# Kernel optimization log

Hardware: AMD Instinct MI355X
Metric: run time of the kernel (lower is better)

The kernel has to match this reference:

```python
import jax, jax.numpy as jnp
import numpy as np

B, T, C = 2, 2048, 2048
NH, NKV, D = 16, 4, 128
N_REP = NH // NKV
THETA = 10000.0


def setup_inputs() -> dict:
    key = jax.random.key(0)
    ks = jax.random.split(key, 5)
    s = 0.02
    return {
        "x": jax.random.normal(ks[0], (B, T, C), dtype=jnp.float32),
        "Wq": jax.random.normal(ks[1], (C, C), dtype=jnp.float32) * s,
        "Wk": jax.random.normal(ks[2], (NKV * D, C), dtype=jnp.float32) * s,
        "Wv": jax.random.normal(ks[3], (NKV * D, C), dtype=jnp.float32) * s,
        "Wo": jax.random.normal(ks[4], (C, C), dtype=jnp.float32) * s,
    }


def _rope(t):
    # t: (B, H, T, D); rotate pairs (even, odd) by angle pos * theta_i
    inv_freq = 1.0 / (THETA ** (jnp.arange(0, D, 2, dtype=jnp.float32) / D))  # (D/2,)
    ang = jnp.arange(T, dtype=jnp.float32)[:, None] * inv_freq[None, :]       # (T, D/2)
    cos, sin = jnp.cos(ang), jnp.sin(ang)
    te, to = t[..., 0::2], t[..., 1::2]
    re = te * cos - to * sin
    ro = te * sin + to * cos
    return jnp.stack([re, ro], axis=-1).reshape(t.shape).astype(t.dtype)


def reference(x, Wq, Wk, Wv, Wo):
    # Projections (Linear: y = x @ W.T)
    q = (x @ Wq.T).reshape(B, T, NH, D).transpose(0, 2, 1, 3)    # (B,NH,T,D)
    k = (x @ Wk.T).reshape(B, T, NKV, D).transpose(0, 2, 1, 3)   # (B,NKV,T,D)
    v = (x @ Wv.T).reshape(B, T, NKV, D).transpose(0, 2, 1, 3)
    q = _rope(q)
    k = _rope(k)
    # GQA: group query heads per kv head instead of materializing repeated K/V
    qg = q.reshape(B, NKV, N_REP, T, D)                          # (B,G,R,T,D)
    scale = 1.0 / jnp.sqrt(jnp.float32(D))
    scores = jnp.einsum("bgrtd,bgsd->bgrts", qg, k) * scale      # (B,G,R,T,T)
    causal = jnp.tril(jnp.ones((T, T), dtype=bool))
    scores = jnp.where(causal, scores, jnp.finfo(scores.dtype).min)
    attn = jax.nn.softmax(scores, axis=-1)
    out = jnp.einsum("bgrts,bgsd->bgrtd", attn, v)               # (B,G,R,T,D)
    out = out.reshape(B, NH, T, D).transpose(0, 2, 1, 3).reshape(B, T, C)
    return out @ Wo.T
```

## Files before the change

kernel.cpp:

```cpp
#include <hip/hip_runtime.h>
#include <hip/hip_bf16.h>
#include <stdint.h>

#define B_   2
#define T_   2048
#define C_   2048
#define NH_  16
#define NKV_ 4
#define D_   128
#define NREP_ 4

typedef __attribute__((ext_vector_type(8))) short bf16x8;
typedef __attribute__((ext_vector_type(4))) float f32x4;

__device__ inline short f2bs(float f) {
    __hip_bfloat16 h = __float2bfloat16(f);
    return *reinterpret_cast<short*>(&h);
}

__device__ inline void gl_lds16(const __hip_bfloat16* g, __hip_bfloat16* l) {
    __builtin_amdgcn_global_load_lds(
        (const __attribute__((address_space(1))) unsigned int*)g,
        (__attribute__((address_space(3))) unsigned int*)l,
        16, 0, 0);
}

__global__ void prep_kernel(const float* __restrict__ x,  const float* __restrict__ Wq,
                            const float* __restrict__ Wk, const float* __restrict__ Wv,
                            const float* __restrict__ Wo,
                            __hip_bfloat16* __restrict__ xb, __hip_bfloat16* __restrict__ wcat,
                            __hip_bfloat16* __restrict__ wob, float2* __restrict__ ropeTab) {
    int tid = blockIdx.x * blockDim.x + threadIdx.x;
    const int CVT_THREADS = 4718592;
    if (tid < CVT_THREADS) {
        int i4 = tid * 4;
        const float* src;
        __hip_bfloat16* dst;
        int off;
        if (i4 < 8388608)       { src = x;  dst = xb;             off = i4; }
        else if (i4 < 12582912) { src = Wq; dst = wcat;           off = i4 - 8388608; }
        else if (i4 < 13631488) { src = Wk; dst = wcat + 4194304; off = i4 - 12582912; }
        else if (i4 < 14680064) { src = Wv; dst = wcat + 5242880; off = i4 - 13631488; }
        else                    { src = Wo; dst = wob;            off = i4 - 14680064; }
        float4 v = *reinterpret_cast<const float4*>(src + off);
        short4 o;
        o.x = f2bs(v.x); o.y = f2bs(v.y); o.z = f2bs(v.z); o.w = f2bs(v.w);
        *reinterpret_cast<short4*>(dst + off) = o;
    } else {
        int e = tid - CVT_THREADS;
        if (e < 131072) {
            int t = e >> 6, p = e & 63;
            float inv = __expf(-(float)p * (9.210340371976184f / 64.0f));
            float ang = (float)t * inv;
            ropeTab[e] = make_float2(cosf(ang), sinf(ang));
        }
    }
}

__global__ __launch_bounds__(256) void gemm_qkv(const __hip_bfloat16* __restrict__ A,
                                                const __hip_bfloat16* __restrict__ Bm,
                                                const float2* __restrict__ ropeTab,
                                                __hip_bfloat16* __restrict__ qo,
                                                __hip_bfloat16* __restrict__ ko,
                                                __hip_bfloat16* __restrict__ vT) {
    const int K = 2048;
    __shared__ __hip_bfloat16 As[128 * 32];
    __shared__ __hip_bfloat16 Bs[128 * 32];
    const int tid  = threadIdx.x;
    const int lane = tid & 63;
    const int wv   = tid >> 6;
    const int m0 = blockIdx.y * 128, n0 = blockIdx.x * 128;
    const int wm = (wv >> 1) * 64, wn = (wv & 1) * 64;
    const int q16 = lane >> 4, r16 = lane & 15;

    f32x4 acc[4][4] = {};

    const int lrow = tid >> 2;
    const int lcol = (tid & 3) * 8;
    const __hip_bfloat16* aG = A  + (size_t)(m0 + lrow) * K + lcol;
    const __hip_bfloat16* bG = Bm + (size_t)(n0 + lrow) * K + lcol;
    __hip_bfloat16* aL = As + tid * 8;
    __hip_bfloat16* bL = Bs + tid * 8;

    for (int k0 = 0; k0 < K; k0 += 32) {
        __syncthreads();
        gl_lds16(aG + k0,          aL);
        gl_lds16(aG + 64 * K + k0, aL + 2048);
        gl_lds16(bG + k0,          bL);
        gl_lds16(bG + 64 * K + k0, bL + 2048);
        __syncthreads();
        bf16x8 af[4], bfr[4];
#pragma unroll
        for (int i = 0; i < 4; i++)
            af[i] = *reinterpret_cast<const bf16x8*>(As + (wm + i * 16 + r16) * 32 + q16 * 8);
#pragma unroll
        for (int j = 0; j < 4; j++)
            bfr[j] = *reinterpret_cast<const bf16x8*>(Bs + (wn + j * 16 + r16) * 32 + q16 * 8);
#pragma unroll
        for (int i = 0; i < 4; i++)
#pragma unroll
            for (int j = 0; j < 4; j++)
                acc[i][j] = __builtin_amdgcn_mfma_f32_16x16x32_bf16(af[i], bfr[j], acc[i][j], 0, 0, 0);
    }

    const int hb = n0 >> 7;
    const float sgn = (r16 & 1) ? 1.0f : -1.0f;
#pragma unroll
    for (int i = 0; i < 4; i++)
#pragma unroll
        for (int r = 0; r < 4; r++) {
            const int m = m0 + wm + i * 16 + q16 * 4 + r;
            const int b = m >> 11, t = m & 2047;
            if (hb < 20) {
                const float2* tabRow = ropeTab + t * 64;
                __hip_bfloat16* dst = (hb < 16)
                    ? qo + ((size_t)(b * NH_ + hb) * T_ + t) * D_
                    : ko + ((size_t)(b * NKV_ + (hb - 16)) * T_ + t) * D_;
#pragma unroll
                for (int j = 0; j < 4; j++) {
                    const int dloc = wn + j * 16 + r16;
                    float v = acc[i][j][r];
                    float prt = __shfl_xor(v, 1);
                    float2 cs = tabRow[dloc >> 1];
                    float res = fmaf(prt * sgn, cs.y, v * cs.x);
                    dst[dloc] = __float2bfloat16(res);
                }
            } else {
                __hip_bfloat16* dst = vT + (size_t)(b * NKV_ + (hb - 20)) * D_ * T_ + t;
#pragma unroll
                for (int j = 0; j < 4; j++) {
                    const int d = wn + j * 16 + r16;
                    dst[(size_t)d * T_] = __float2bfloat16(acc[i][j][r]);
                }
            }
        }
}

template <int MODE, int BN, int NTN>
__global__ __launch_bounds__(512, 2) void gemm_ff(
    const __hip_bfloat16* __restrict__ A,
    const __hip_bfloat16* __restrict__ Bm,
    const float2* __restrict__ ropeTab,
    __hip_bfloat16* __restrict__ qo,
    __hip_bfloat16* __restrict__ ko,
    __hip_bfloat16* __restrict__ vT,
    float* __restrict__ Cout) {
    constexpr int K = 2048;
    constexpr int NT = K / 64;
    constexpr int WN = BN / 64;
    constexpr int WM = 8 / WN;
    constexpr int RPW = 256 / WM;
    constexpr int MI_T = RPW / 16;
    constexpr int BSZ = BN * 64;
    constexpr int BLOADS = BSZ / 8192;
    extern __shared__ char lds[];

    const int tid = threadIdx.x;
    const int lane = tid & 63;
    const int wid = tid >> 6;
    const int wm = wid / WN, wn = wid % WN;
    const int q16 = lane >> 4, r16 = lane & 15;

    const int cpx = (int)gridDim.x >> 3;
    const int bs = ((int)blockIdx.x & 7) * cpx + ((int)blockIdx.x >> 3);
    const int tm = bs / NTN, tn = bs % NTN;
    const int rmA = tm * 256, rmB = tn * BN;

    const int csw = (q16 << 4) ^ ((r16 & 3) << 4);

    f32x4 acc[MI_T][4] = {};
    bf16x8 aF[MI_T], bF[4];

#define STG_A(buf_, sl_, kstep_)                                                     \
    { _Pragma("unroll") for (int li = 0; li < 2; li++) {                             \
        const int L_ = li * 8192 + tid * 16;                                         \
        const int rw_ = L_ >> 6;                                                     \
        const int cb_ = (L_ & 63) ^ ((rw_ & 3) << 4);                                \
        gl_lds16(A + (size_t)(rmA + rw_) * K + (kstep_) * 64 + (sl_) * 32 + (cb_ >> 1), \
                 (__hip_bfloat16*)(lds + (buf_) * 32768 + (sl_) * 16384 + L_));      \
    } }
#define STG_B(buf_, sl_, kstep_)                                                     \
    { _Pragma("unroll") for (int li = 0; li < BLOADS; li++) {                        \
        const int L_ = li * 8192 + tid * 16;                                         \
        const int rw_ = L_ >> 6;                                                     \
        const int cb_ = (L_ & 63) ^ ((rw_ & 3) << 4);                                \
        gl_lds16(Bm + (size_t)(rmB + rw_) * K + (kstep_) * 64 + (sl_) * 32 + (cb_ >> 1), \
                 (__hip_bfloat16*)(lds + 65536 + (buf_) * 2 * BSZ + (sl_) * BSZ + L_)); \
    } }
#define RD_A(buf_, sl_)                                                              \
    { _Pragma("unroll") for (int mi = 0; mi < MI_T; mi++)                            \
        aF[mi] = *(const bf16x8*)(lds + (buf_) * 32768 + (sl_) * 16384 +             \
                                  (wm * RPW + mi * 16 + r16) * 64 + csw); }
#define RD_B(buf_, sl_)                                                              \
    { _Pragma("unroll") for (int bi = 0; bi < 4; bi++)                               \
        bF[bi] = *(const bf16x8*)(lds + 65536 + (buf_) * 2 * BSZ + (sl_) * BSZ +     \
                                  (wn * 64 + bi * 16 + r16) * 64 + csw); }
#define MM_                                                                          \
    { __builtin_amdgcn_s_setprio(1);                                                 \
      _Pragma("unroll") for (int mi = 0; mi < MI_T; mi++)                            \
      _Pragma("unroll") for (int bi = 0; bi < 4; bi++)                               \
          acc[mi][bi] = __builtin_amdgcn_mfma_f32_16x16x32_bf16(                     \
              aF[mi], bF[bi], acc[mi][bi], 0, 0, 0);                                 \
      __builtin_amdgcn_s_setprio(0); }
#define VMC                                                                          \
    { if constexpr (BLOADS == 2) { asm volatile("s_waitcnt vmcnt(4)" ::: "memory"); } \
      else                       { asm volatile("s_waitcnt vmcnt(3)" ::: "memory"); } }
#define BAR __builtin_amdgcn_s_barrier()

    STG_A(0, 0, 0); STG_B(0, 0, 0);
    STG_A(0, 1, 0); STG_B(0, 1, 0);
    VMC; BAR;

    for (int u = 0; u < NT - 1; u++) {
        const int bf_ = u & 1;
        RD_A(bf_, 0); RD_B(bf_, 0);
        STG_A(bf_ ^ 1, 0, u + 1); STG_B(bf_ ^ 1, 0, u + 1);
        MM_;
        VMC; BAR;
        RD_A(bf_, 1); RD_B(bf_, 1);
        STG_A(bf_ ^ 1, 1, u + 1); STG_B(bf_ ^ 1, 1, u + 1);
        MM_;
        VMC; BAR;
    }
    {
        const int bf_ = (NT - 1) & 1;
        RD_A(bf_, 0); RD_B(bf_, 0);
        MM_;
        asm volatile("s_waitcnt vmcnt(0)" ::: "memory"); BAR;
        RD_A(bf_, 1); RD_B(bf_, 1);
        MM_;
    }
#undef BAR
#undef VMC
#undef MM_
#undef RD_B
#undef RD_A
#undef STG_B
#undef STG_A

    if constexpr (MODE == 0) {
        constexpr int N = NTN * BN;
        float* const cbase = Cout + (size_t)(rmA + wm * RPW) * N + tn * BN + wn * 64 + r16;
#pragma unroll
        for (int mi = 0; mi < MI_T; mi++)
#pragma unroll
            for (int r = 0; r < 4; r++) {
                float* dst = cbase + (size_t)(mi * 16 + q16 * 4 + r) * N;
#pragma unroll
                for (int bi = 0; bi < 4; bi++)
                    dst[bi * 16] = acc[mi][bi][r];
            }
    } else {
        const int hb = tn * 2 + (wn >> 1);
        const float sgn = (r16 & 1) ? 1.0f : -1.0f;
#pragma unroll
        for (int mi = 0; mi < MI_T; mi++)
#pragma unroll
            for (int r = 0; r < 4; r++) {
                const int m = rmA + wm * RPW + mi * 16 + q16 * 4 + r;
                const int bb = m >> 11, t = m & 2047;
                if (hb < 20) {
                    const float2* tabRow = ropeTab + t * 64;
                    __hip_bfloat16* dst = (hb < 16)
                        ? qo + ((size_t)(bb * NH_ + hb) * T_ + t) * D_
                        : ko + ((size_t)(bb * NKV_ + (hb - 16)) * T_ + t) * D_;
#pragma unroll
                    for (int bi = 0; bi < 4; bi++) {
                        const int dloc = (wn & 1) * 64 + bi * 16 + r16;
                        float v = acc[mi][bi][r];
                        float prt = __shfl_xor(v, 1);
                        float2 cs = tabRow[dloc >> 1];
                        dst[dloc] = __float2bfloat16(fmaf(prt * sgn, cs.y, v * cs.x));
                    }
                } else {
                    __hip_bfloat16* dst = vT + (size_t)(bb * NKV_ + (hb - 20)) * D_ * T_ + t;
#pragma unroll
                    for (int bi = 0; bi < 4; bi++) {
                        const int dloc = (wn & 1) * 64 + bi * 16 + r16;
                        dst[(size_t)dloc * T_] = __float2bfloat16(acc[mi][bi][r]);
                    }
                }
            }
    }
}

__global__ __launch_bounds__(256, 3) void attn_kernel(const __hip_bfloat16* __restrict__ Q,
                                                      const __hip_bfloat16* __restrict__ Kt,
                                                      const __hip_bfloat16* __restrict__ Vt,
                                                      __hip_bfloat16* __restrict__ Ao,
                                                      float* __restrict__ O0,
                                                      float* __restrict__ O1,
                                                      float* __restrict__ l0p,
                                                      float* __restrict__ l1p) {
    __shared__ __hip_bfloat16 Ks[2][4096];
    __shared__ __hip_bfloat16 Vs[2][4096];
    __shared__ __hip_bfloat16 Pl[4][1280];

    const int lane = threadIdx.x & 63, wv = threadIdx.x >> 6;
    const int bg = blockIdx.y;
    const int u  = (int)blockIdx.x;
    int tb, nIt, sIdx;
    if (u < 32)      { tb = u;      nIt = tb + 1;      sIdx = -1; }
    else if (u < 64) { tb = u;      nIt = 32;          sIdx = 0;  }
    else             { tb = u - 32; nIt = tb + 1 - 32; sIdx = 1;  }
    const int sBase = (sIdx == 1) ? 1024 : 0;
    const int b = bg >> 2, g = bg & 3;
    const int h = g * 4 + wv;
    const int t0 = tb * 32;
    const int q16 = lane >> 4, r16 = lane & 15;

    const __hip_bfloat16* qh = Q + ((size_t)((b * NH_ + h) * T_) + t0) * D_;
    const __hip_bfloat16* kh = Kt + (size_t)(b * NKV_ + g) * T_ * D_;
    const __hip_bfloat16* vh = Vt + (size_t)(b * NKV_ + g) * D_ * T_;

    bf16x8 bqA[4], bqB[4];
#pragma unroll
    for (int kk = 0; kk < 4; kk++) {
        bqA[kk] = *reinterpret_cast<const bf16x8*>(qh + (size_t)r16 * D_ + kk * 32 + q16 * 8);
        bqB[kk] = *reinterpret_cast<const bf16x8*>(qh + (size_t)(16 + r16) * D_ + kk * 32 + q16 * 8);
    }

    float liA = 0.f, liB = 0.f;
    f32x4 oA[8], oB[8];
#pragma unroll
    for (int d = 0; d < 8; d++) {
        oA[d] = (f32x4){0.f, 0.f, 0.f, 0.f};
        oB[d] = (f32x4){0.f, 0.f, 0.f, 0.f};
    }

    const float SCL2 = 0.088388347648318447f * 1.4426950408889634f;
    const int tqA = t0 + r16;
    const int tqB = t0 + 16 + r16;

    const __hip_bfloat16* gK = kh + (size_t)((wv & 1) * 16 + r16) * D_ + q16 * 8;
    const __hip_bfloat16* gV = vh + (size_t)(((wv - 2) * 4) * 16 + r16) * T_ + q16 * 8;

#define STAGE(bufi, s0_)                                                        \
    do {                                                                        \
        if (wv < 2) {                                                           \
            const __hip_bfloat16* gp = gK + (size_t)(s0_) * D_;                 \
            __hip_bfloat16* lp = &Ks[bufi][(wv * 4) * 512] + lane * 8;          \
            gl_lds16(gp,      lp);                                              \
            gl_lds16(gp + 32, lp + 512);                                        \
            gl_lds16(gp + 64, lp + 1024);                                      \
            gl_lds16(gp + 96, lp + 1536);                                      \
        } else {                                                                \
            const __hip_bfloat16* gp = gV + (s0_);                              \
            __hip_bfloat16* lp = &Vs[bufi][((wv - 2) * 4) * 512] + lane * 8;    \
            gl_lds16(gp,                      lp);                              \
            gl_lds16(gp + (size_t)16 * T_,    lp + 512);                        \
            gl_lds16(gp + (size_t)32 * T_,    lp + 1024);                      \
            gl_lds16(gp + (size_t)48 * T_,    lp + 1536);                      \
        }                                                                       \
    } while (0)

    STAGE(0, sBase);

    for (int j = 0; j < nIt; j++) {
        const int s0 = sBase + j * 32;
        const int cur = j & 1;
        __syncthreads();
        if (j + 1 < nIt) STAGE(cur ^ 1, s0 + 32);

        f32x4 sc0A = (f32x4){0.f, 0.f, 0.f, 0.f};
        f32x4 sc1A = (f32x4){0.f, 0.f, 0.f, 0.f};
        f32x4 sc0B = (f32x4){0.f, 0.f, 0.f, 0.f};
        f32x4 sc1B = (f32x4){0.f, 0.f, 0.f, 0.f};
        {
            bf16x8 ak[4];
#pragma unroll
            for (int kk = 0; kk < 4; kk++)
                ak[kk] = *reinterpret_cast<const bf16x8*>(&Ks[cur][kk * 512] + lane * 8);
#pragma unroll
            for (int kk = 0; kk < 4; kk++) {
                sc0A = __builtin_amdgcn_mfma_f32_16x16x32_bf16(ak[kk], bqA[kk], sc0A, 0, 0, 0);
                sc0B = __builtin_amdgcn_mfma_f32_16x16x32_bf16(ak[kk], bqB[kk], sc0B, 0, 0, 0);
            }
#pragma unroll
            for (int kk = 0; kk < 4; kk++)
                ak[kk] = *reinterpret_cast<const bf16x8*>(&Ks[cur][(4 + kk) * 512] + lane * 8);
#pragma unroll
            for (int kk = 0; kk < 4; kk++) {
                sc1A = __builtin_amdgcn_mfma_f32_16x16x32_bf16(ak[kk], bqA[kk], sc1A, 0, 0, 0);
                sc1B = __builtin_amdgcn_mfma_f32_16x16x32_bf16(ak[kk], bqB[kk], sc1B, 0, 0, 0);
            }
        }

        ushort4 w0A, w1A, w0B, w1B;
        float psA = 0.f, psB = 0.f;
        if (s0 + 32 > t0) {
#pragma unroll
            for (int r = 0; r < 4; r++) {
                int s_a = s0 + q16 * 4 + r;
                float pa0 = (s_a <= tqA)      ? __builtin_amdgcn_exp2f(sc0A[r] * SCL2) : 0.f;
                float pa1 = (s_a + 16 <= tqA) ? __builtin_amdgcn_exp2f(sc1A[r] * SCL2) : 0.f;
                float pb0 = (s_a <= tqB)      ? __builtin_amdgcn_exp2f(sc0B[r] * SCL2) : 0.f;
                float pb1 = (s_a + 16 <= tqB) ? __builtin_amdgcn_exp2f(sc1B[r] * SCL2) : 0.f;
                psA += pa0 + pa1;
                psB += pb0 + pb1;
                ((unsigned short*)&w0A)[r] = (unsigned short)f2bs(pa0);
                ((unsigned short*)&w1A)[r] = (unsigned short)f2bs(pa1);
                ((unsigned short*)&w0B)[r] = (unsigned short)f2bs(pb0);
                ((unsigned short*)&w1B)[r] = (unsigned short)f2bs(pb1);
            }
        } else {
#pragma unroll
            for (int r = 0; r < 4; r++) {
                float pa0 = __builtin_amdgcn_exp2f(sc0A[r] * SCL2);
                float pa1 = __builtin_amdgcn_exp2f(sc1A[r] * SCL2);
                float pb0 = __builtin_amdgcn_exp2f(sc0B[r] * SCL2);
                float pb1 = __builtin_amdgcn_exp2f(sc1B[r] * SCL2);
                psA += pa0 + pa1;
                psB += pb0 + pb1;
                ((unsigned short*)&w0A)[r] = (unsigned short)f2bs(pa0);
                ((unsigned short*)&w1A)[r] = (unsigned short)f2bs(pa1);
                ((unsigned short*)&w0B)[r] = (unsigned short)f2bs(pb0);
                ((unsigned short*)&w1B)[r] = (unsigned short)f2bs(pb1);
            }
        }
        liA += psA;
        liB += psB;

        *reinterpret_cast<ushort4*>(&Pl[wv][r16 * 40 + q16 * 4]) = w0A;
        *reinterpret_cast<ushort4*>(&Pl[wv][r16 * 40 + 16 + q16 * 4]) = w1A;
        *reinterpret_cast<ushort4*>(&Pl[wv][640 + r16 * 40 + q16 * 4]) = w0B;
        *reinterpret_cast<ushort4*>(&Pl[wv][640 + r16 * 40 + 16 + q16 * 4]) = w1B;
        asm volatile("s_waitcnt lgkmcnt(0)" ::: "memory");
        bf16x8 pfA = *reinterpret_cast<const bf16x8*>(&Pl[wv][r16 * 40 + q16 * 8]);
        bf16x8 pfB = *reinterpret_cast<const bf16x8*>(&Pl[wv][640 + r16 * 40 + q16 * 8]);

#pragma unroll
        for (int d = 0; d < 8; d++) {
            bf16x8 bv = *reinterpret_cast<const bf16x8*>(&Vs[cur][d * 512] + lane * 8);
            oA[d] = __builtin_amdgcn_mfma_f32_16x16x32_bf16(pfA, bv, oA[d], 0, 0, 0);
            oB[d] = __builtin_amdgcn_mfma_f32_16x16x32_bf16(pfB, bv, oB[d], 0, 0, 0);
        }
    }

    liA += __shfl_xor(liA, 16);
    liA += __shfl_xor(liA, 32);
    liB += __shfl_xor(liB, 16);
    liB += __shfl_xor(liB, 32);

    if (sIdx < 0) {
#pragma unroll
        for (int r = 0; r < 4; r++) {
            float lrA = __shfl(liA, q16 * 4 + r, 16);
            float lrB = __shfl(liB, q16 * 4 + r, 16);
            float invA = 1.0f / lrA;
            float invB = 1.0f / lrB;
            int tA = t0 + q16 * 4 + r;
            __hip_bfloat16* dstA = Ao + (size_t)(b * T_ + tA) * C_ + h * D_ + r16;
            __hip_bfloat16* dstB = dstA + (size_t)16 * C_;
#pragma unroll
            for (int d = 0; d < 8; d++) {
                dstA[d * 16] = __float2bfloat16(oA[d][r] * invA);
                dstB[d * 16] = __float2bfloat16(oB[d][r] * invB);
            }
        }
    } else {
        float* Os = (sIdx == 0) ? O0 : O1;
        float* ls = (sIdx == 0) ? l0p : l1p;
        const size_t rb = (size_t)(b * NH_ + h) * 1024 + (size_t)(t0 - 1024);
        if (q16 == 0) {
            ls[rb + r16]      = liA;
            ls[rb + 16 + r16] = liB;
        }
#pragma unroll
        for (int r = 0; r < 4; r++) {
            int rowl = q16 * 4 + r;
            float* dA = Os + (rb + rowl) * 128 + r16;
            float* dB = Os + (rb + 16 + rowl) * 128 + r16;
#pragma unroll
            for (int d = 0; d < 8; d++) {
                dA[d * 16] = oA[d][r];
                dB[d * 16] = oB[d][r];
            }
        }
    }
#undef STAGE
}

__global__ void attn_combine(const float* __restrict__ O0, const float* __restrict__ O1,
                             const float* __restrict__ l0, const float* __restrict__ l1,
                             __hip_bfloat16* __restrict__ Ao) {
    int idx = blockIdx.x * blockDim.x + threadIdx.x;
    int row = idx >> 5, d4 = (idx & 31) << 2;
    int bh = row >> 10, tl = row & 1023;
    int b = bh >> 4, h = bh & 15;
    float inv = 1.0f / (l0[row] + l1[row]);
    float4 a = *reinterpret_cast<const float4*>(O0 + (size_t)row * 128 + d4);
    float4 c = *reinterpret_cast<const float4*>(O1 + (size_t)row * 128 + d4);
    short4 o;
    o.x = f2bs((a.x + c.x) * inv);
    o.y = f2bs((a.y + c.y) * inv);
    o.z = f2bs((a.z + c.z) * inv);
    o.w = f2bs((a.w + c.w) * inv);
    *reinterpret_cast<short4*>(Ao + (size_t)(b * T_ + 1024 + tl) * C_ + h * D_ + d4) = o;
}

extern "C" void kernel_launch(void* const* d_in, const int* in_sizes, int n_in,
                              void* d_out, int out_size, void* d_ws, size_t ws_size,
                              hipStream_t stream) {
    const float* x  = (const float*)d_in[0];
    const float* Wq = (const float*)d_in[1];
    const float* Wk = (const float*)d_in[2];
    const float* Wv = (const float*)d_in[3];
    const float* Wo = (const float*)d_in[4];
    float* out = (float*)d_out;
    char* ws = (char*)d_ws;

    __hip_bfloat16* xb   = (__hip_bfloat16*)(ws + 0);
    __hip_bfloat16* wcat = (__hip_bfloat16*)(ws + 16777216);
    float2*         ropeTab = (float2*)(ws + 29360128);
    __hip_bfloat16* wob  = (__hip_bfloat16*)(ws + 30408704);
    __hip_bfloat16* qatt = (__hip_bfloat16*)(ws + 38797312);
    __hip_bfloat16* katt = (__hip_bfloat16*)(ws + 55574528);
    __hip_bfloat16* vT   = (__hip_bfloat16*)(ws + 59768832);
    __hip_bfloat16* aout = (__hip_bfloat16*)(ws + 63963136);
    float* O0 = (float*)(ws + 0);
    float* O1 = (float*)(ws + 80740352);
    float* l0 = (float*)(ws + 97517568);
    float* l1 = (float*)(ws + 97648640);

    static bool s_attr_done = false;
    if (!s_attr_done) {
        hipFuncSetAttribute(reinterpret_cast<const void*>(&gemm_ff<0, 128, 16>),
                            hipFuncAttributeMaxDynamicSharedMemorySize, 98304);
        s_attr_done = true;
    }

    const int thr = 256;
    prep_kernel<<<18944, thr, 0, stream>>>(x, Wq, Wk, Wv, Wo, xb, wcat, wob, ropeTab);

    gemm_qkv<<<dim3(24, 32), 256, 0, stream>>>(xb, wcat, ropeTab, qatt, katt, vT);

    attn_kernel<<<dim3(96, 8), 256, 0, stream>>>(qatt, katt, vT, aout, O0, O1, l0, l1);
    attn_combine<<<(2 * NH_ * 1024 * 32) / thr, thr, 0, stream>>>(O0, O1, l0, l1, aout);

    gemm_ff<0, 128, 16><<<256, 512, 98304, stream>>>(aout, wob, nullptr, nullptr, nullptr, nullptr, out);
}
```

Measured before the change: 282.9 us.

## Feed P directly to 16x16x16 MFMA, skipping LDS round trip

In attention, P values now stay in registers and go straight into 16x16x16 bf16 MFMAs, which match the accumulator layout of the score MFMA. This removes the per-iteration LDS write, wait and read of P. The cost is twice as many MFMA instructions, each with a smaller K. The causal block ordering is also reversed for the split blocks so long-running blocks schedule first, and the unused QKV epilogue is removed from gemm_ff.

```diff
diff --git a/kernel.cpp b/kernel.cpp
--- a/kernel.cpp
+++ b/kernel.cpp
@@ -11,7 +11,15 @@
 #define NREP_ 4
 
 typedef __attribute__((ext_vector_type(8))) short bf16x8;
+typedef __attribute__((ext_vector_type(4))) short bf16x4;
 typedef __attribute__((ext_vector_type(4))) float f32x4;
+
+#if __has_builtin(__builtin_amdgcn_mfma_f32_16x16x16bf16_1k)
+#define HAVE_MFMA16 1
+#define MFMA16(a, b, c) __builtin_amdgcn_mfma_f32_16x16x16bf16_1k(a, b, c, 0, 0, 0)
+#else
+#define HAVE_MFMA16 0
+#endif
 
 __device__ inline short f2bs(float f) {
     __hip_bfloat16 h = __float2bfloat16(f);
@@ -140,10 +148,6 @@
 __global__ __launch_bounds__(512, 2) void gemm_ff(
     const __hip_bfloat16* __restrict__ A,
     const __hip_bfloat16* __restrict__ Bm,
-    const float2* __restrict__ ropeTab,
-    __hip_bfloat16* __restrict__ qo,
-    __hip_bfloat16* __restrict__ ko,
-    __hip_bfloat16* __restrict__ vT,
     float* __restrict__ Cout) {
     constexpr int K = 2048;
     constexpr int NT = K / 64;
@@ -250,37 +254,6 @@
                 for (int bi = 0; bi < 4; bi++)
                     dst[bi * 16] = acc[mi][bi][r];
             }
-    } else {
-        const int hb = tn * 2 + (wn >> 1);
-        const float sgn = (r16 & 1) ? 1.0f : -1.0f;
-#pragma unroll
-        for (int mi = 0; mi < MI_T; mi++)
-#pragma unroll
-            for (int r = 0; r < 4; r++) {
-                const int m = rmA + wm * RPW + mi * 16 + q16 * 4 + r;
-                const int bb = m >> 11, t = m & 2047;
-                if (hb < 20) {
-                    const float2* tabRow = ropeTab + t * 64;
-                    __hip_bfloat16* dst = (hb < 16)
-                        ? qo + ((size_t)(bb * NH_ + hb) * T_ + t) * D_
-                        : ko + ((size_t)(bb * NKV_ + (hb - 16)) * T_ + t) * D_;
-#pragma unroll
-                    for (int bi = 0; bi < 4; bi++) {
-                        const int dloc = (wn & 1) * 64 + bi * 16 + r16;
-                        float v = acc[mi][bi][r];
-                        float prt = __shfl_xor(v, 1);
-                        float2 cs = tabRow[dloc >> 1];
-                        dst[dloc] = __float2bfloat16(fmaf(prt * sgn, cs.y, v * cs.x));
-                    }
-                } else {
-                    __hip_bfloat16* dst = vT + (size_t)(bb * NKV_ + (hb - 20)) * D_ * T_ + t;
-#pragma unroll
-                    for (int bi = 0; bi < 4; bi++) {
-                        const int dloc = (wn & 1) * 64 + bi * 16 + r16;
-                        dst[(size_t)dloc * T_] = __float2bfloat16(acc[mi][bi][r]);
-                    }
-                }
-            }
     }
 }
 
@@ -294,15 +267,17 @@
                                                       float* __restrict__ l1p) {
     __shared__ __hip_bfloat16 Ks[2][4096];
     __shared__ __hip_bfloat16 Vs[2][4096];
+#if !HAVE_MFMA16
     __shared__ __hip_bfloat16 Pl[4][1280];
+#endif
 
     const int lane = threadIdx.x & 63, wv = threadIdx.x >> 6;
     const int bg = blockIdx.y;
-    const int u  = (int)blockIdx.x;
+    const int xb_ = (int)blockIdx.x;
     int tb, nIt, sIdx;
-    if (u < 32)      { tb = u;      nIt = tb + 1;      sIdx = -1; }
-    else if (u < 64) { tb = u;      nIt = 32;          sIdx = 0;  }
-    else             { tb = u - 32; nIt = tb + 1 - 32; sIdx = 1;  }
+    if (xb_ < 32)      { tb = xb_;       nIt = xb_ + 1;  sIdx = -1; }
+    else if (xb_ < 64) { tb = 95 - xb_;  nIt = 32;       sIdx = 0;  }
+    else               { tb = 127 - xb_; nIt = 96 - xb_; sIdx = 1;  }
     const int sBase = (sIdx == 1) ? 1024 : 0;
     const int b = bg >> 2, g = bg & 3;
     const int h = g * 4 + wv;
@@ -331,6 +306,9 @@
     const float SCL2 = 0.088388347648318447f * 1.4426950408889634f;
     const int tqA = t0 + r16;
     const int tqB = t0 + 16 + r16;
+#if HAVE_MFMA16
+    const int vIdx = (q16 >> 1) * 128 + r16 * 8 + (q16 & 1) * 4;
+#endif
 
     const __hip_bfloat16* gK = kh + (size_t)((wv & 1) * 16 + r16) * D_ + q16 * 8;
     const __hip_bfloat16* gV = vh + (size_t)(((wv - 2) * 4) * 16 + r16) * T_ + q16 * 8;
@@ -342,15 +320,15 @@
             __hip_bfloat16* lp = &Ks[bufi][(wv * 4) * 512] + lane * 8;          \
             gl_lds16(gp,      lp);                                              \
             gl_lds16(gp + 32, lp + 512);                                        \
-            gl_lds16(gp + 64, lp + 1024);                                      \
-            gl_lds16(gp + 96, lp + 1536);                                      \
+            gl_lds16(gp + 64, lp + 1024);                                       \
+            gl_lds16(gp + 96, lp + 1536);                                       \
         } else {                                                                \
             const __hip_bfloat16* gp = gV + (s0_);                              \
             __hip_bfloat16* lp = &Vs[bufi][((wv - 2) * 4) * 512] + lane * 8;    \
             gl_lds16(gp,                      lp);                              \
             gl_lds16(gp + (size_t)16 * T_,    lp + 512);                        \
-            gl_lds16(gp + (size_t)32 * T_,    lp + 1024);                      \
-            gl_lds16(gp + (size_t)48 * T_,    lp + 1536);                      \
+            gl_lds16(gp + (size_t)32 * T_,    lp + 1024);                       \
+            gl_lds16(gp + (size_t)48 * T_,    lp + 1536);                       \
         }                                                                       \
     } while (0)
 
@@ -386,41 +364,60 @@
             }
         }
 
-        ushort4 w0A, w1A, w0B, w1B;
         float psA = 0.f, psB = 0.f;
         if (s0 + 32 > t0) {
 #pragma unroll
             for (int r = 0; r < 4; r++) {
                 int s_a = s0 + q16 * 4 + r;
-                float pa0 = (s_a <= tqA)      ? __builtin_amdgcn_exp2f(sc0A[r] * SCL2) : 0.f;
-                float pa1 = (s_a + 16 <= tqA) ? __builtin_amdgcn_exp2f(sc1A[r] * SCL2) : 0.f;
-                float pb0 = (s_a <= tqB)      ? __builtin_amdgcn_exp2f(sc0B[r] * SCL2) : 0.f;
-                float pb1 = (s_a + 16 <= tqB) ? __builtin_amdgcn_exp2f(sc1B[r] * SCL2) : 0.f;
-                psA += pa0 + pa1;
-                psB += pb0 + pb1;
-                ((unsigned short*)&w0A)[r] = (unsigned short)f2bs(pa0);
-                ((unsigned short*)&w1A)[r] = (unsigned short)f2bs(pa1);
-                ((unsigned short*)&w0B)[r] = (unsigned short)f2bs(pb0);
-                ((unsigned short*)&w1B)[r] = (unsigned short)f2bs(pb1);
+                sc0A[r] = (s_a <= tqA)      ? __builtin_amdgcn_exp2f(sc0A[r] * SCL2) : 0.f;
+                sc1A[r] = (s_a + 16 <= tqA) ? __builtin_amdgcn_exp2f(sc1A[r] * SCL2) : 0.f;
+                sc0B[r] = (s_a <= tqB)      ? __builtin_amdgcn_exp2f(sc0B[r] * SCL2) : 0.f;
+                sc1B[r] = (s_a + 16 <= tqB) ? __builtin_amdgcn_exp2f(sc1B[r] * SCL2) : 0.f;
+                psA += sc0A[r] + sc1A[r];
+                psB += sc0B[r] + sc1B[r];
             }
         } else {
 #pragma unroll
             for (int r = 0; r < 4; r++) {
-                float pa0 = __builtin_amdgcn_exp2f(sc0A[r] * SCL2);
-                float pa1 = __builtin_amdgcn_exp2f(sc1A[r] * SCL2);
-                float pb0 = __builtin_amdgcn_exp2f(sc0B[r] * SCL2);
-                float pb1 = __builtin_amdgcn_exp2f(sc1B[r] * SCL2);
-                psA += pa0 + pa1;
-                psB += pb0 + pb1;
-                ((unsigned short*)&w0A)[r] = (unsigned short)f2bs(pa0);
-                ((unsigned short*)&w1A)[r] = (unsigned short)f2bs(pa1);
-                ((unsigned short*)&w0B)[r] = (unsigned short)f2bs(pb0);
-                ((unsigned short*)&w1B)[r] = (unsigned short)f2bs(pb1);
+                sc0A[r] = __builtin_amdgcn_exp2f(sc0A[r] * SCL2);
+                sc1A[r] = __builtin_amdgcn_exp2f(sc1A[r] * SCL2);
+                sc0B[r] = __builtin_amdgcn_exp2f(sc0B[r] * SCL2);
+                sc1B[r] = __builtin_amdgcn_exp2f(sc1B[r] * SCL2);
+                psA += sc0A[r] + sc1A[r];
+                psB += sc0B[r] + sc1B[r];
             }
         }
         liA += psA;
         liB += psB;
 
+#if HAVE_MFMA16
+        bf16x4 pf0A, pf1A, pf0B, pf1B;
+#pragma unroll
+        for (int r = 0; r < 4; r++) {
+            pf0A[r] = f2bs(sc0A[r]);
+            pf1A[r] = f2bs(sc1A[r]);
+            pf0B[r] = f2bs(sc0B[r]);
+            pf1B[r] = f2bs(sc1B[r]);
+        }
+        const __hip_bfloat16* vbase = &Vs[cur][vIdx];
+#pragma unroll
+        for (int d = 0; d < 8; d++) {
+            bf16x4 bvlo = *reinterpret_cast<const bf16x4*>(vbase + d * 512);
+            bf16x4 bvhi = *reinterpret_cast<const bf16x4*>(vbase + d * 512 + 256);
+            oA[d] = MFMA16(pf0A, bvlo, oA[d]);
+            oA[d] = MFMA16(pf1A, bvhi, oA[d]);
+            oB[d] = MFMA16(pf0B, bvlo, oB[d]);
+            oB[d] = MFMA16(pf1B, bvhi, oB[d]);
+        }
+#else
+        ushort4 w0A, w1A, w0B, w1B;
+#pragma unroll
+        for (int r = 0; r < 4; r++) {
+            ((unsigned short*)&w0A)[r] = (unsigned short)f2bs(sc0A[r]);
+            ((unsigned short*)&w1A)[r] = (unsigned short)f2bs(sc1A[r]);
+            ((unsigned short*)&w0B)[r] = (unsigned short)f2bs(sc0B[r]);
+            ((unsigned short*)&w1B)[r] = (unsigned short)f2bs(sc1B[r]);
+        }
         *reinterpret_cast<ushort4*>(&Pl[wv][r16 * 40 + q16 * 4]) = w0A;
         *reinterpret_cast<ushort4*>(&Pl[wv][r16 * 40 + 16 + q16 * 4]) = w1A;
         *reinterpret_cast<ushort4*>(&Pl[wv][640 + r16 * 40 + q16 * 4]) = w0B;
@@ -428,13 +425,13 @@
         asm volatile("s_waitcnt lgkmcnt(0)" ::: "memory");
         bf16x8 pfA = *reinterpret_cast<const bf16x8*>(&Pl[wv][r16 * 40 + q16 * 8]);
         bf16x8 pfB = *reinterpret_cast<const bf16x8*>(&Pl[wv][640 + r16 * 40 + q16 * 8]);
-
 #pragma unroll
         for (int d = 0; d < 8; d++) {
             bf16x8 bv = *reinterpret_cast<const bf16x8*>(&Vs[cur][d * 512] + lane * 8);
             oA[d] = __builtin_amdgcn_mfma_f32_16x16x32_bf16(pfA, bv, oA[d], 0, 0, 0);
             oB[d] = __builtin_amdgcn_mfma_f32_16x16x32_bf16(pfB, bv, oB[d], 0, 0, 0);
         }
+#endif
     }
 
     liA += __shfl_xor(liA, 16);
@@ -538,5 +535,5 @@
     attn_kernel<<<dim3(96, 8), 256, 0, stream>>>(qatt, katt, vT, aout, O0, O1, l0, l1);
     attn_combine<<<(2 * NH_ * 1024 * 32) / thr, thr, 0, stream>>>(O0, O1, l0, l1, aout);
 
-    gemm_ff<0, 128, 16><<<256, 512, 98304, stream>>>(aout, wob, nullptr, nullptr, nullptr, nullptr, out);
-}
+    gemm_ff<0, 128, 16><<<256, 512, 98304, stream>>>(aout, wob, out);
+}
```

New measurement: 281.7 us. About the same (-0.4%).
